# Kernel optimization log

Hardware: AMD Instinct MI355X
Metric: run time of the kernel (lower is better)

The kernel has to match this reference:

```python
import math
import jax, jax.numpy as jnp
import numpy as np

BATCH = 16384
N = 2048            # in_size = out_size, power of 2
LOG_N = 11          # log2(N)
NSTACKS = 1
NBLOCKS = 1


def setup_inputs() -> dict:
    key = jax.random.key(0)
    k1, k2, k3 = jax.random.split(key, 3)
    x = jax.random.normal(k1, (BATCH, N), jnp.float32)
    # init='randn': twiddle ~ N(0,1) / sqrt(2)
    twiddle = jax.random.normal(
        k2, (NSTACKS, NBLOCKS, LOG_N, N // 2, 2, 2), jnp.float32) / jnp.sqrt(jnp.float32(2.0))
    bound = 1.0 / math.sqrt(N)  # nn.Linear-style bias init, in_size = N
    bias = jax.random.uniform(k3, (N,), jnp.float32, -bound, bound)
    return {"x": x, "twiddle": twiddle, "bias": bias}


def butterfly_multiply(twiddle, x, increasing_stride=True):
    # twiddle: (S, n_blocks, log_n, n//2, 2, 2);  x: (B, S, n)
    B, S, n = x.shape
    n_blocks, log_n = twiddle.shape[1], twiddle.shape[2]
    out = x
    cur = increasing_stride
    for block in range(n_blocks):
        for idx in range(log_n):
            log_stride = idx if cur else log_n - 1 - idx
            s = 1 << log_stride
            g = n // (2 * s)  # number of butterfly groups at this stride
            # t: (S, g, s, 2, 2); pair axis j contracts against input halves
            t = twiddle[:, block, idx].reshape(S, g, s, 2, 2)
            xr = out.reshape(B, S, g, 2, s)
            out = jnp.einsum('kgsij,bkgjs->bkgis', t, xr).reshape(B, S, n)
        cur = not cur
    return out


def reference(x, twiddle, bias):
    B = x.shape[0]
    # pre_process: flatten batch dims, expand over nstacks
    out = jnp.broadcast_to(x[:, None, :], (B, NSTACKS, N))
    out = butterfly_multiply(twiddle, out, increasing_stride=True)
    # post_process: flatten stacks, truncate to out_size, add bias
    out = out.reshape(B, NSTACKS * N)[:, :N] + bias
    return out
```

## Files before the change

### kernel.cpp

```cpp
#include <hip/hip_runtime.h>


constexpr int BATCH = 16384;
constexpr int N = 2048;
constexpr int ROWS = 2;
constexpr int WPB = 4;
constexpr int BLOCK = 64 * WPB;

__global__ __launch_bounds__(BLOCK, 2)
void butterfly_kernel(const float* __restrict__ x,
                      const float* __restrict__ tw,
                      const float* __restrict__ bias,
                      float* __restrict__ out)
{
    const int lane = threadIdx.x & 63;
    const int wid  = blockIdx.x * WPB + (threadIdx.x >> 6);
    const size_t row0 = (size_t)wid * ROWS;
    const int l2 = lane * 2;

    float v[ROWS][32];

    #pragma unroll
    for (int rr = 0; rr < ROWS; ++rr) {
        const float* src = x + (row0 + rr) * N + l2;
        #pragma unroll
        for (int r = 0; r < 16; ++r) {
            const float2 f = *(const float2*)(src + r * 128);
            v[rr][2*r]   = f.x;
            v[rr][2*r+1] = f.y;
        }
    }

    #pragma unroll
    for (int r = 0; r < 16; ++r) {
        const int p = r * 64 + lane;
        const float4 t4 = *(const float4*)(tw + 4 * p);
        #pragma unroll
        for (int rr = 0; rr < ROWS; ++rr) {
            const float lo = v[rr][2*r];
            const float hi = v[rr][2*r+1];
            v[rr][2*r]   = fmaf(t4.x, lo, t4.y * hi);
            v[rr][2*r+1] = fmaf(t4.z, lo, t4.w * hi);
        }
    }

    #pragma unroll
    for (int st = 1; st < 7; ++st) {
        const int s = 1 << st;
        const int m = 1 << (st - 1);
        const int hiHalf = (lane >> (st - 1)) & 1;
        const float* twst = tw + (st << 12);
        #pragma unroll
        for (int k = 0; k < 32; ++k) {
            const int e = (k >> 1) * 128 + l2 + (k & 1);
            const int p = ((e >> (st + 1)) << st) | (e & (s - 1));
            const float2 t2 = *(const float2*)(twst + 4 * p + 2 * hiHalf);
            #pragma unroll
            for (int rr = 0; rr < ROWS; ++rr) {
                const float mine = v[rr][k];
                const float part = __shfl_xor(mine, m, 64);
                const float lo = hiHalf ? part : mine;
                const float hi = hiHalf ? mine : part;
                v[rr][k] = fmaf(t2.x, lo, t2.y * hi);
            }
        }
    }

    #pragma unroll
    for (int st = 7; st < 11; ++st) {
        const int s = 1 << st;
        const int rm = 1 << (st - 7);
        const float* twst = tw + (st << 12);
        #pragma unroll
        for (int r = 0; r < 16; ++r) {
            if (r & rm) continue;
            #pragma unroll
            for (int j = 0; j < 2; ++j) {
                const int e = r * 128 + l2 + j;
                const int p = ((e >> (st + 1)) << st) | (e & (s - 1));
                const float4 t4 = *(const float4*)(twst + 4 * p);
                const int klo = 2 * r + j;
                const int khi = 2 * (r + rm) + j;
                #pragma unroll
                for (int rr = 0; rr < ROWS; ++rr) {
                    const float lo = v[rr][klo];
                    const float hi = v[rr][khi];
                    v[rr][klo] = fmaf(t4.x, lo, t4.y * hi);
                    v[rr][khi] = fmaf(t4.z, lo, t4.w * hi);
                }
            }
        }
    }

    #pragma unroll
    for (int r = 0; r < 16; ++r) {
        const float2 b = *(const float2*)(bias + r * 128 + l2);
        #pragma unroll
        for (int rr = 0; rr < ROWS; ++rr) {
            float2 o;
            o.x = v[rr][2*r]   + b.x;
            o.y = v[rr][2*r+1] + b.y;
            *(float2*)(out + (row0 + rr) * N + r * 128 + l2) = o;
        }
    }
}

extern "C" void kernel_launch(void* const* d_in, const int* in_sizes, int n_in,
                              void* d_out, int out_size, void* d_ws, size_t ws_size,
                              hipStream_t stream) {
    const float* x    = (const float*)d_in[0];
    const float* tw   = (const float*)d_in[1];
    const float* bias = (const float*)d_in[2];
    float* out = (float*)d_out;

    const int rows_per_block = ROWS * WPB;
    const int grid = BATCH / rows_per_block;
    butterfly_kernel<<<grid, BLOCK, 0, stream>>>(x, tw, bias, out);
}
```

Before: 296.0 us.

## Stage twiddles through double-buffered LDS, use DPP/swizzle shuffles, four rows per wave

Each stage's twiddle block is copied into a double-buffered, bank-swizzled LDS region with direct global-to-LDS loads, prefetching the next stage while the current one computes. The per-lane twiddle global loads are replaced by LDS reads. Cross-lane exchanges for small strides now use DPP and ds_swizzle in place of generic shuffles. Rows per wave go from two to four to spread each twiddle read over more rows. This costs block-wide barriers per stage, more register pressure (up to 128 live values), and an occupancy target raised to 3 that may cause spills.

```diff
diff --git a/kernel.cpp b/kernel.cpp
--- a/kernel.cpp
+++ b/kernel.cpp
@@ -3,20 +3,107 @@
 
 constexpr int BATCH = 16384;
 constexpr int N = 2048;
-constexpr int ROWS = 2;
+constexpr int ROWS = 4;
 constexpr int WPB = 4;
 constexpr int BLOCK = 64 * WPB;
+constexpr int GRID = BATCH / (ROWS * WPB);
 
-__global__ __launch_bounds__(BLOCK, 2)
+__device__ __forceinline__ int swz(int a) { return a ^ (((a >> 5) & 1) << 2); }
+
+template <int M>
+__device__ __forceinline__ float part_xor(float x) {
+    if constexpr (M == 1)
+        return __int_as_float(__builtin_amdgcn_mov_dpp(__float_as_int(x), 0xB1, 0xF, 0xF, true));
+    else if constexpr (M == 2)
+        return __int_as_float(__builtin_amdgcn_mov_dpp(__float_as_int(x), 0x4E, 0xF, 0xF, true));
+    else if constexpr (M == 4)
+        return __int_as_float(__builtin_amdgcn_ds_swizzle(__float_as_int(x), 0x101F));
+    else if constexpr (M == 8)
+        return __int_as_float(__builtin_amdgcn_ds_swizzle(__float_as_int(x), 0x201F));
+    else if constexpr (M == 16)
+        return __int_as_float(__builtin_amdgcn_ds_swizzle(__float_as_int(x), 0x401F));
+    else
+        return __shfl_xor(x, 32, 64);
+}
+
+template <int ST>
+__device__ __forceinline__ void mid_stage(float (&v)[ROWS][32], const float* twb, int lane) {
+    constexpr int s = 1 << ST;
+    constexpr int m = 1 << (ST - 1);
+    const int hiHalf = (lane >> (ST - 1)) & 1;
+    const int l2 = lane * 2;
+    #pragma unroll
+    for (int k = 0; k < 32; ++k) {
+        const int e = (k >> 1) * 128 + l2 + (k & 1);
+        const int p = ((e >> (ST + 1)) << ST) | (e & (s - 1));
+        const int a = swz(4 * p + 2 * hiHalf);
+        const float2 t2 = *(const float2*)(twb + a);
+        #pragma unroll
+        for (int rr = 0; rr < ROWS; ++rr) {
+            const float mine = v[rr][k];
+            const float part = part_xor<m>(mine);
+            const float lo = hiHalf ? part : mine;
+            const float hi = hiHalf ? mine : part;
+            v[rr][k] = fmaf(t2.x, lo, t2.y * hi);
+        }
+    }
+}
+
+template <int ST>
+__device__ __forceinline__ void hi_stage(float (&v)[ROWS][32], const float* twb, int lane) {
+    constexpr int s = 1 << ST;
+    constexpr int rm = 1 << (ST - 7);
+    const int l2 = lane * 2;
+    #pragma unroll
+    for (int r = 0; r < 16; ++r) {
+        if (r & rm) continue;
+        #pragma unroll
+        for (int j = 0; j < 2; ++j) {
+            const int e = r * 128 + l2 + j;
+            const int p = ((e >> (ST + 1)) << ST) | (e & (s - 1));
+            const int a = swz(4 * p);
+            const float4 t4 = *(const float4*)(twb + a);
+            const int klo = 2 * r + j;
+            const int khi = 2 * (r + rm) + j;
+            #pragma unroll
+            for (int rr = 0; rr < ROWS; ++rr) {
+                const float lo = v[rr][klo];
+                const float hi = v[rr][khi];
+                v[rr][klo] = fmaf(t4.x, lo, t4.y * hi);
+                v[rr][khi] = fmaf(t4.z, lo, t4.w * hi);
+            }
+        }
+    }
+}
+
+__global__ __launch_bounds__(BLOCK, 3)
 void butterfly_kernel(const float* __restrict__ x,
                       const float* __restrict__ tw,
                       const float* __restrict__ bias,
                       float* __restrict__ out)
 {
-    const int lane = threadIdx.x & 63;
-    const int wid  = blockIdx.x * WPB + (threadIdx.x >> 6);
+    __shared__ __align__(16) float lds[2][4096];
+    const int tid = threadIdx.x;
+    const int lane = tid & 63;
+    const int w = tid >> 6;
+    const int wid = blockIdx.x * WPB + w;
     const size_t row0 = (size_t)wid * ROWS;
     const int l2 = lane * 2;
+
+    auto stage_tw = [&](int st, int buf) {
+        const float* base = tw + (st << 12);
+        #pragma unroll
+        for (int i = 0; i < 4; ++i) {
+            const int s = i * 256 + (w << 6) + lane;
+            const int g = s ^ ((s >> 3) & 1);
+            __builtin_amdgcn_global_load_lds(
+                (const __attribute__((address_space(1))) void*)(base + 4 * g),
+                (__attribute__((address_space(3))) void*)(&lds[buf][(i * 256 + (w << 6)) * 4]),
+                16, 0, 0);
+        }
+    };
+
+    stage_tw(1, 1);
 
     float v[ROWS][32];
 
@@ -33,8 +120,7 @@
 
     #pragma unroll
     for (int r = 0; r < 16; ++r) {
-        const int p = r * 64 + lane;
-        const float4 t4 = *(const float4*)(tw + 4 * p);
+        const float4 t4 = *(const float4*)(tw + 4 * (r * 64 + lane));
         #pragma unroll
         for (int rr = 0; rr < ROWS; ++rr) {
             const float lo = v[rr][2*r];
@@ -43,54 +129,18 @@
             v[rr][2*r+1] = fmaf(t4.z, lo, t4.w * hi);
         }
     }
+    __syncthreads();
 
-    #pragma unroll
-    for (int st = 1; st < 7; ++st) {
-        const int s = 1 << st;
-        const int m = 1 << (st - 1);
-        const int hiHalf = (lane >> (st - 1)) & 1;
-        const float* twst = tw + (st << 12);
-        #pragma unroll
-        for (int k = 0; k < 32; ++k) {
-            const int e = (k >> 1) * 128 + l2 + (k & 1);
-            const int p = ((e >> (st + 1)) << st) | (e & (s - 1));
-            const float2 t2 = *(const float2*)(twst + 4 * p + 2 * hiHalf);
-            #pragma unroll
-            for (int rr = 0; rr < ROWS; ++rr) {
-                const float mine = v[rr][k];
-                const float part = __shfl_xor(mine, m, 64);
-                const float lo = hiHalf ? part : mine;
-                const float hi = hiHalf ? mine : part;
-                v[rr][k] = fmaf(t2.x, lo, t2.y * hi);
-            }
-        }
-    }
-
-    #pragma unroll
-    for (int st = 7; st < 11; ++st) {
-        const int s = 1 << st;
-        const int rm = 1 << (st - 7);
-        const float* twst = tw + (st << 12);
-        #pragma unroll
-        for (int r = 0; r < 16; ++r) {
-            if (r & rm) continue;
-            #pragma unroll
-            for (int j = 0; j < 2; ++j) {
-                const int e = r * 128 + l2 + j;
-                const int p = ((e >> (st + 1)) << st) | (e & (s - 1));
-                const float4 t4 = *(const float4*)(twst + 4 * p);
-                const int klo = 2 * r + j;
-                const int khi = 2 * (r + rm) + j;
-                #pragma unroll
-                for (int rr = 0; rr < ROWS; ++rr) {
-                    const float lo = v[rr][klo];
-                    const float hi = v[rr][khi];
-                    v[rr][klo] = fmaf(t4.x, lo, t4.y * hi);
-                    v[rr][khi] = fmaf(t4.z, lo, t4.w * hi);
-                }
-            }
-        }
-    }
+    stage_tw(2, 0);  mid_stage<1>(v, &lds[1][0], lane); __syncthreads();
+    stage_tw(3, 1);  mid_stage<2>(v, &lds[0][0], lane); __syncthreads();
+    stage_tw(4, 0);  mid_stage<3>(v, &lds[1][0], lane); __syncthreads();
+    stage_tw(5, 1);  mid_stage<4>(v, &lds[0][0], lane); __syncthreads();
+    stage_tw(6, 0);  mid_stage<5>(v, &lds[1][0], lane); __syncthreads();
+    stage_tw(7, 1);  mid_stage<6>(v, &lds[0][0], lane); __syncthreads();
+    stage_tw(8, 0);  hi_stage<7>(v, &lds[1][0], lane);  __syncthreads();
+    stage_tw(9, 1);  hi_stage<8>(v, &lds[0][0], lane);  __syncthreads();
+    stage_tw(10, 0); hi_stage<9>(v, &lds[1][0], lane);  __syncthreads();
+    hi_stage<10>(v, &lds[0][0], lane);
 
     #pragma unroll
     for (int r = 0; r < 16; ++r) {
@@ -113,7 +163,5 @@
     const float* bias = (const float*)d_in[2];
     float* out = (float*)d_out;
 
-    const int rows_per_block = ROWS * WPB;
-    const int grid = BATCH / rows_per_block;
-    butterfly_kernel<<<grid, BLOCK, 0, stream>>>(x, tw, bias, out);
+    butterfly_kernel<<<GRID, BLOCK, 0, stream>>>(x, tw, bias, out);
 }
```

New measurement: 448.0 us. 51.4% more time.
